# Kernel optimization log

Hardware: AMD Instinct MI355X
Metric: run time of the kernel (lower is better)

The kernel has to match this reference:

```python
import jax, jax.numpy as jnp
import numpy as np
from functools import partial

BIG = 1e9  # placeholder squared distance for 'no surface voxel here'


def _surface(fg):
    """Boundary voxels: foreground with at least one 4-neighbor background (image border counts as background)."""
    p = jnp.pad(fg, 1)  # pads with False
    interior = p[:-2, 1:-1] & p[2:, 1:-1] & p[1:-1, :-2] & p[1:-1, 2:]
    return fg & ~interior


def _edt(mask):
    """Exact Euclidean distance transform (unit spacing, matching spacing_mm=(1,1,1)).
    Separable two-pass: 1D squared distance along rows, then combine along columns.
    mask: [H, W] bool -> dist: [H, W] float32 distance to nearest True voxel."""
    H, W = mask.shape
    i = jnp.arange(H, dtype=jnp.float32)
    j = jnp.arange(W, dtype=jnp.float32)
    d1 = (i[:, None] - i[None, :]) ** 2                      # [H, H]
    pen = jnp.where(mask, 0.0, BIG).astype(jnp.float32)      # [H, W]
    g = jnp.min(d1[:, :, None] + pen[None, :, :], axis=1)    # [H, W] (min over source row i')
    d2 = (j[:, None] - j[None, :]) ** 2                      # [W, W]
    f = jnp.min(g[:, None, :] + d2[None, :, :], axis=2)      # [H, W] (min over source col j')
    return jnp.sqrt(f)


def _percentile(d, mask, pct):
    """pct-percentile of d over voxels where mask is True (inf if mask empty)."""
    vals = jnp.sort(jnp.where(mask, d, jnp.inf).ravel())
    n = jnp.sum(mask)
    idx = jnp.clip(jnp.ceil(pct / 100.0 * n.astype(jnp.float32)).astype(jnp.int32) - 1,
                   0, vals.size - 1)
    return jnp.where(n > 0, vals[idx], jnp.inf)


def _pair_hd(pred_m, gt_m):
    """Robust Hausdorff (100th and 95th percentile) between surfaces of two binary masks."""
    sp = _surface(pred_m)
    sg = _surface(gt_m)
    dt_to_pred = _edt(sp)  # distance of every voxel to pred surface
    dt_to_gt = _edt(sg)    # distance of every voxel to gt surface

    def robust(p):
        return jnp.maximum(_percentile(dt_to_pred, sg, p),   # gt -> pred
                           _percentile(dt_to_gt, sp, p))     # pred -> gt

    return jnp.stack([robust(100.0), robust(95.0)])  # [2]


def _forward(logits, target):
    num_classes = logits.shape[1]
    probs = jax.nn.softmax(logits, axis=1)
    pred = jnp.argmax(probs, axis=1)  # [B, H, W]
    classes = jnp.arange(1, num_classes)  # include_background=False -> drop class 0
    pred_oh = pred[:, None, :, :] == classes[None, :, None, None]    # [B, Cfg, H, W] bool
    tgt_oh = target[:, None, :, :] == classes[None, :, None, None]   # [B, Cfg, H, W] bool

    def per_image(args):
        pm, tm = args  # each [Cfg, H, W]
        return jax.vmap(_pair_hd)(pm, tm)  # [Cfg, 2]

    res = jax.lax.map(per_image, (pred_oh, tgt_oh))  # [B, Cfg, 2]
    # average='micro': mean over all (batch, class) pairs
    return jnp.mean(res, axis=(0, 1))  # [2] = (hd100, hd95)


def setup_inputs() -> dict:
    key = jax.random.key(0)
    k1, k2 = jax.random.split(key)
    B, C, H, W = 8, 4, 192, 192
    logits = jax.random.normal(k1, (B, C, H, W), dtype=jnp.float32)
    target = jax.random.randint(k2, (B, H, W), 0, C, dtype=jnp.int64)
    return {"logits": logits, "target": target}


def reference(logits, target):
    return _forward(logits, target)
```

## Files before the change

### kernel.cpp

```cpp
#include <hip/hip_runtime.h>
#include <hip/hip_bf16.h>
#include <math.h>
#include <stdint.h>
#include <limits.h>

#define BB 8
#define NC 4
#define HH 192
#define WW 192
#define HWP (HH * WW)
#define NPAIR 24
#define NPD 48
#define NWRD 576
#define NCHUNK 16
#define WPC (NWRD / NCHUNK)
#define BIGI 1000000000

typedef unsigned long long u64;

__global__ void k_prep(const float* __restrict__ logits, const int* __restrict__ target,
                       u64* __restrict__ fgbits) {
    int idx = blockIdx.x * 256 + threadIdx.x;
    int b = idx / HWP;
    int p = idx - b * HWP;
    const float* base = logits + (size_t)b * NC * HWP + p;
    float l0 = base[0], l1 = base[HWP], l2 = base[2 * HWP], l3 = base[3 * HWP];
    int pred = 0; float best = l0;
    if (l1 > best) { best = l1; pred = 1; }
    if (l2 > best) { best = l2; pred = 2; }
    if (l3 > best) { best = l3; pred = 3; }
    int t = target[(size_t)b * HWP + p];
    int lane = threadIdx.x & 63;
    int g = p >> 6;
#pragma unroll
    for (int cls = 1; cls <= 3; ++cls) {
        u64 mp = __ballot(pred == cls);
        u64 mt = __ballot(t == cls);
        if (lane == 0) {
            int pair = b * 3 + (cls - 1);
            fgbits[(size_t)(pair * 2 + 0) * NWRD + g] = mp;
            fgbits[(size_t)(pair * 2 + 1) * NWRD + g] = mt;
        }
    }
}

__device__ __forceinline__ u64 surf_word(const u64* F, int i, int k) {
    u64 r0 = F[i * 3], r1 = F[i * 3 + 1], r2 = F[i * 3 + 2];
    u64 r = F[i * 3 + k];
    u64 u = (i > 0) ? F[(i - 1) * 3 + k] : 0ull;
    u64 d = (i < HH - 1) ? F[(i + 1) * 3 + k] : 0ull;
    u64 lf, rt;
    if (k == 0)      { lf = r0 << 1;                rt = (r0 >> 1) | (r1 << 63); }
    else if (k == 1) { lf = (r1 << 1) | (r0 >> 63); rt = (r1 >> 1) | (r2 << 63); }
    else             { lf = (r2 << 1) | (r1 >> 63); rt = r2 >> 1; }
    return r & ~(u & d & lf & rt);
}

__device__ __forceinline__ int rowdist(const u64* w, int j) {
    int qw = j >> 6, qb = j & 63;
    int dr = INT_MAX, dl = INT_MAX;
    u64 m = w[qw] & (~0ull << qb);
    if (m) dr = ((qw << 6) + __ffsll(m) - 1) - j;
    else {
        for (int k = qw + 1; k < 3; ++k)
            if (w[k]) { dr = ((k << 6) + __ffsll(w[k]) - 1) - j; break; }
    }
    u64 ml = w[qw] & (~0ull >> (63 - qb));
    if (ml) dl = j - ((qw << 6) + 63 - __clzll((long long)ml));
    else {
        for (int k = qw - 1; k >= 0; --k)
            if (w[k]) { dl = j - ((k << 6) + 63 - __clzll((long long)w[k])); break; }
    }
    return min(dl, dr);
}

__global__ __launch_bounds__(256) void k_query(const u64* __restrict__ fgbits,
                        int* __restrict__ list, int* __restrict__ cnt) {
    int chunk = blockIdx.x, pd = blockIdx.y, qpd = pd ^ 1;
    int tid = threadIdx.x;
    __shared__ u64 sF[NWRD];
    __shared__ u64 sG[NWRD];
    __shared__ u64 sS[NWRD];
    __shared__ uint16_t qb[WPC * 64];
    __shared__ int wcnt[WPC + 1];
    __shared__ int sbase;

    for (int t = tid; t < NWRD; t += 256) {
        sF[t] = fgbits[(size_t)pd * NWRD + t];
        sG[t] = fgbits[(size_t)qpd * NWRD + t];
    }
    __syncthreads();

    for (int w = tid; w < NWRD; w += 256) sS[w] = surf_word(sF, w / 3, w % 3);

    u64 myq = 0;
    if (tid < WPC) {
        int w = chunk * WPC + tid;
        myq = surf_word(sG, w / 3, w % 3);
        wcnt[tid] = __popcll(myq);
    }
    __syncthreads();
    if (tid == 0) {
        int acc = 0;
        for (int w = 0; w < WPC; ++w) { int c = wcnt[w]; wcnt[w] = acc; acc += c; }
        wcnt[WPC] = acc;
        sbase = atomicAdd(&cnt[pd], acc);
    }
    __syncthreads();
    if (tid < WPC) {
        int w = chunk * WPC + tid;
        int i = w / 3, k = w % 3;
        int off = wcnt[tid];
        u64 m = myq;
        while (m) { int bi = __ffsll(m) - 1; m &= m - 1; qb[off++] = (uint16_t)((i << 8) | (k * 64 + bi)); }
    }
    __syncthreads();

    int nq = wcnt[WPC], base = sbase;
    for (int q = tid; q < nq; q += 256) {
        int e = qb[q];
        int qi = e >> 8, qj = e & 255;
        int best = BIGI;
        for (int s = 0; s < HH; ++s) {
            if (s * s >= best) break;
            int r = qi - s;
            if (r >= 0) {
                int dj = rowdist(sS + r * 3, qj);
                if (dj != INT_MAX) best = min(best, s * s + dj * dj);
            }
            r = qi + s;
            if (s > 0 && r < HH) {
                int dj = rowdist(sS + r * 3, qj);
                if (dj != INT_MAX) best = min(best, s * s + dj * dj);
            }
        }
        list[(size_t)pd * HWP + base + q] = best;
    }
}

__global__ __launch_bounds__(1024) void k_pick(const int* __restrict__ list,
                        const int* __restrict__ cnt, float* __restrict__ res) {
    int pd = blockIdx.x, tid = threadIdx.x;
    int n = cnt[pd];
    const int* L = list + (size_t)pd * HWP;
    int lv[16];
#pragma unroll
    for (int t = 0; t < 16; ++t) {
        int k = tid + t * 1024;
        lv[t] = (k < n) ? L[k] : INT_MAX;
    }
    __shared__ int sw[16];
    __shared__ int stot;

    int lmax = -1;
#pragma unroll
    for (int t = 0; t < 16; ++t) if (lv[t] != INT_MAX) lmax = max(lmax, lv[t]);
    for (int off = 32; off; off >>= 1) lmax = max(lmax, __shfl_down(lmax, off));
    if ((tid & 63) == 0) sw[tid >> 6] = lmax;
    __syncthreads();
    if (tid == 0) { int m = -1; for (int w = 0; w < 16; ++w) m = max(m, sw[w]); stot = m; }
    __syncthreads();
    int vmax = stot;
    __syncthreads();

    int kk;
    { float kf = ceilf(0.95f * (float)n); kk = (int)kf; if (kk < 1) kk = 1; if (kk > n) kk = n; }

    int lo = 0, hi = min(vmax, 72962);
    while (lo < hi) {
        int mid = (lo + hi) >> 1;
        int c = 0;
#pragma unroll
        for (int t = 0; t < 16; ++t) if (lv[t] <= mid) c++;
        for (int off = 32; off; off >>= 1) c += __shfl_down(c, off);
        if ((tid & 63) == 0) sw[tid >> 6] = c;
        __syncthreads();
        if (tid == 0) { int s = 0; for (int w = 0; w < 16; ++w) s += sw[w]; stot = s; }
        __syncthreads();
        if (stot >= kk) hi = mid; else lo = mid + 1;
        __syncthreads();
    }
    int c = 0;
#pragma unroll
    for (int t = 0; t < 16; ++t) if (lv[t] <= lo) c++;
    for (int off = 32; off; off >>= 1) c += __shfl_down(c, off);
    if ((tid & 63) == 0) sw[tid >> 6] = c;
    __syncthreads();
    if (tid == 0) {
        int s = 0; for (int w = 0; w < 16; ++w) s += sw[w];
        int v95 = (n > 0 && s >= kk) ? lo : BIGI;
        float r100, r95;
        if (n == 0) { r100 = INFINITY; r95 = INFINITY; }
        else { r100 = sqrtf((float)vmax); r95 = sqrtf((float)v95); }
        res[pd * 2 + 0] = r100;
        res[pd * 2 + 1] = r95;
    }
}

__global__ void k_final(const float* __restrict__ res, float* __restrict__ out) {
    int tid = threadIdx.x;
    float v100 = 0.0f, v95 = 0.0f;
    if (tid < NPAIR) {
        v100 = fmaxf(res[tid * 4 + 0], res[tid * 4 + 2]);
        v95  = fmaxf(res[tid * 4 + 1], res[tid * 4 + 3]);
    }
    for (int off = 32; off; off >>= 1) {
        v100 += __shfl_down(v100, off);
        v95  += __shfl_down(v95, off);
    }
    if (tid == 0) {
        out[0] = v100 / (float)NPAIR;
        out[1] = v95 / (float)NPAIR;
    }
}

extern "C" void kernel_launch(void* const* d_in, const int* in_sizes, int n_in,
                              void* d_out, int out_size, void* d_ws, size_t ws_size,
                              hipStream_t stream) {
    const float* logits = (const float*)d_in[0];
    const int* target = (const int*)d_in[1];
    float* out = (float*)d_out;

    uint8_t* ws = (uint8_t*)d_ws;
    u64*   fgbits = (u64*)ws;
    int*   list   = (int*)(ws + 221184);
    int*   cnt    = (int*)(ws + 7299072);
    float* res    = (float*)(ws + 7299264);

    hipMemsetAsync(cnt, 0, NPD * sizeof(int), stream);

    k_prep<<<(BB * HWP) / 256, 256, 0, stream>>>(logits, target, fgbits);
    k_query<<<dim3(NCHUNK, NPD), 256, 0, stream>>>(fgbits, list, cnt);
    k_pick<<<NPD, 1024, 0, stream>>>(list, cnt, res);
    k_final<<<1, 64, 0, stream>>>(res, out);
}
```

Before: 82.28 us.

## Fuse all stages into one cooperative persistent kernel with grid syncs

Replaces the memset and four separate launches with a single cooperative kernel of 768 blocks that runs the prep, query, percentile-pick and final-reduce stages, separated by grid.sync. The goal is to remove launch gaps and the memset. The pick stage now uses 256-thread blocks and stages the per-pair distance list in shared memory, falling back to global memory beyond the cap. Risks are the cost of grid-wide barriers, fewer threads working in the pick phase, and occupancy limits from the larger shared-memory union needed to keep 768 blocks co-resident.

After: 289.1 us. 3.51x slower.

```diff
diff --git a/kernel.cpp b/kernel.cpp
--- a/kernel.cpp
+++ b/kernel.cpp
@@ -1,8 +1,11 @@
 #include <hip/hip_runtime.h>
+#include <hip/hip_cooperative_groups.h>
 #include <hip/hip_bf16.h>
 #include <math.h>
 #include <stdint.h>
 #include <limits.h>
+
+namespace cg = cooperative_groups;
 
 #define BB 8
 #define NC 4
@@ -14,35 +17,25 @@
 #define NWRD 576
 #define NCHUNK 16
 #define WPC (NWRD / NCHUNK)
+#define GB 768
+#define PCAP 12288
 #define BIGI 1000000000
 
 typedef unsigned long long u64;
 
-__global__ void k_prep(const float* __restrict__ logits, const int* __restrict__ target,
-                       u64* __restrict__ fgbits) {
-    int idx = blockIdx.x * 256 + threadIdx.x;
-    int b = idx / HWP;
-    int p = idx - b * HWP;
-    const float* base = logits + (size_t)b * NC * HWP + p;
-    float l0 = base[0], l1 = base[HWP], l2 = base[2 * HWP], l3 = base[3 * HWP];
-    int pred = 0; float best = l0;
-    if (l1 > best) { best = l1; pred = 1; }
-    if (l2 > best) { best = l2; pred = 2; }
-    if (l3 > best) { best = l3; pred = 3; }
-    int t = target[(size_t)b * HWP + p];
-    int lane = threadIdx.x & 63;
-    int g = p >> 6;
-#pragma unroll
-    for (int cls = 1; cls <= 3; ++cls) {
-        u64 mp = __ballot(pred == cls);
-        u64 mt = __ballot(t == cls);
-        if (lane == 0) {
-            int pair = b * 3 + (cls - 1);
-            fgbits[(size_t)(pair * 2 + 0) * NWRD + g] = mp;
-            fgbits[(size_t)(pair * 2 + 1) * NWRD + g] = mt;
-        }
-    }
-}
+struct P2 {
+    u64 sF[NWRD];
+    u64 sG[NWRD];
+    u64 sS[NWRD];
+    uint16_t qb[WPC * 64];
+    int wcnt[WPC + 1];
+    int sbase;
+};
+struct P3 {
+    int vals[PCAP];
+    int sw[4];
+};
+union ShU { P2 p2; P3 p3; };
 
 __device__ __forceinline__ u64 surf_word(const u64* F, int i, int k) {
     u64 r0 = F[i * 3], r1 = F[i * 3 + 1], r2 = F[i * 3 + 2];
@@ -57,15 +50,15 @@
 }
 
 __device__ __forceinline__ int rowdist(const u64* w, int j) {
-    int qw = j >> 6, qb = j & 63;
+    int qw = j >> 6, qb2 = j & 63;
     int dr = INT_MAX, dl = INT_MAX;
-    u64 m = w[qw] & (~0ull << qb);
+    u64 m = w[qw] & (~0ull << qb2);
     if (m) dr = ((qw << 6) + __ffsll(m) - 1) - j;
     else {
         for (int k = qw + 1; k < 3; ++k)
             if (w[k]) { dr = ((k << 6) + __ffsll(w[k]) - 1) - j; break; }
     }
-    u64 ml = w[qw] & (~0ull >> (63 - qb));
+    u64 ml = w[qw] & (~0ull >> (63 - qb2));
     if (ml) dl = j - ((qw << 6) + 63 - __clzll((long long)ml));
     else {
         for (int k = qw - 1; k >= 0; --k)
@@ -74,143 +67,174 @@
     return min(dl, dr);
 }
 
-__global__ __launch_bounds__(256) void k_query(const u64* __restrict__ fgbits,
-                        int* __restrict__ list, int* __restrict__ cnt) {
-    int chunk = blockIdx.x, pd = blockIdx.y, qpd = pd ^ 1;
-    int tid = threadIdx.x;
-    __shared__ u64 sF[NWRD];
-    __shared__ u64 sG[NWRD];
-    __shared__ u64 sS[NWRD];
-    __shared__ uint16_t qb[WPC * 64];
-    __shared__ int wcnt[WPC + 1];
-    __shared__ int sbase;
-
-    for (int t = tid; t < NWRD; t += 256) {
-        sF[t] = fgbits[(size_t)pd * NWRD + t];
-        sG[t] = fgbits[(size_t)qpd * NWRD + t];
-    }
-    __syncthreads();
-
-    for (int w = tid; w < NWRD; w += 256) sS[w] = surf_word(sF, w / 3, w % 3);
-
-    u64 myq = 0;
-    if (tid < WPC) {
-        int w = chunk * WPC + tid;
-        myq = surf_word(sG, w / 3, w % 3);
-        wcnt[tid] = __popcll(myq);
-    }
-    __syncthreads();
-    if (tid == 0) {
-        int acc = 0;
-        for (int w = 0; w < WPC; ++w) { int c = wcnt[w]; wcnt[w] = acc; acc += c; }
-        wcnt[WPC] = acc;
-        sbase = atomicAdd(&cnt[pd], acc);
-    }
-    __syncthreads();
-    if (tid < WPC) {
-        int w = chunk * WPC + tid;
-        int i = w / 3, k = w % 3;
-        int off = wcnt[tid];
-        u64 m = myq;
-        while (m) { int bi = __ffsll(m) - 1; m &= m - 1; qb[off++] = (uint16_t)((i << 8) | (k * 64 + bi)); }
-    }
-    __syncthreads();
-
-    int nq = wcnt[WPC], base = sbase;
-    for (int q = tid; q < nq; q += 256) {
-        int e = qb[q];
-        int qi = e >> 8, qj = e & 255;
-        int best = BIGI;
-        for (int s = 0; s < HH; ++s) {
-            if (s * s >= best) break;
-            int r = qi - s;
-            if (r >= 0) {
-                int dj = rowdist(sS + r * 3, qj);
-                if (dj != INT_MAX) best = min(best, s * s + dj * dj);
+__device__ __forceinline__ void prep_word(int w, int lane, const float* __restrict__ logits,
+                                          const int* __restrict__ target, u64* __restrict__ fgbits) {
+    int b = w / NWRD;
+    int g = w - b * NWRD;
+    int p = (g << 6) + lane;
+    const float* base = logits + (size_t)b * NC * HWP + p;
+    float l0 = base[0], l1 = base[HWP], l2 = base[2 * HWP], l3 = base[3 * HWP];
+    int pred = 0; float best = l0;
+    if (l1 > best) { best = l1; pred = 1; }
+    if (l2 > best) { best = l2; pred = 2; }
+    if (l3 > best) { best = l3; pred = 3; }
+    int t = target[(size_t)b * HWP + p];
+#pragma unroll
+    for (int cls = 1; cls <= 3; ++cls) {
+        u64 mp = __ballot(pred == cls);
+        u64 mt = __ballot(t == cls);
+        if (lane == 0) {
+            int pair = b * 3 + (cls - 1);
+            fgbits[(size_t)(pair * 2 + 0) * NWRD + g] = mp;
+            fgbits[(size_t)(pair * 2 + 1) * NWRD + g] = mt;
+        }
+    }
+}
+
+__device__ __forceinline__ int block_reduce_add(int v, int* sw, int tid) {
+    for (int off = 32; off; off >>= 1) v += __shfl_down(v, off);
+    if ((tid & 63) == 0) sw[tid >> 6] = v;
+    __syncthreads();
+    int r = sw[0] + sw[1] + sw[2] + sw[3];
+    __syncthreads();
+    return r;
+}
+__device__ __forceinline__ int block_reduce_max(int v, int* sw, int tid) {
+    for (int off = 32; off; off >>= 1) v = max(v, __shfl_down(v, off));
+    if ((tid & 63) == 0) sw[tid >> 6] = v;
+    __syncthreads();
+    int r = max(max(sw[0], sw[1]), max(sw[2], sw[3]));
+    __syncthreads();
+    return r;
+}
+
+__global__ __launch_bounds__(256, 3) void k_all(const float* __restrict__ logits,
+                        const int* __restrict__ target, u64* __restrict__ fgbits,
+                        int* __restrict__ list, int* __restrict__ cnt,
+                        float* __restrict__ res, float* __restrict__ out) {
+    cg::grid_group grid = cg::this_grid();
+    __shared__ ShU sh;
+    int tid = threadIdx.x, bid = blockIdx.x;
+
+    if (bid == 0 && tid < NPD) cnt[tid] = 0;
+    {
+        int gtid = bid * 256 + tid;
+        int w0 = gtid >> 6, lane = gtid & 63;
+        prep_word(w0, lane, logits, target, fgbits);
+        int w1 = w0 + 3072;
+        if (w1 < BB * NWRD) prep_word(w1, lane, logits, target, fgbits);
+    }
+    grid.sync();
+
+    {
+        int pd = bid >> 4, chunk = bid & 15, qpd = pd ^ 1;
+        for (int t = tid; t < NWRD; t += 256) {
+            sh.p2.sF[t] = fgbits[(size_t)pd * NWRD + t];
+            sh.p2.sG[t] = fgbits[(size_t)qpd * NWRD + t];
+        }
+        __syncthreads();
+        for (int w = tid; w < NWRD; w += 256) sh.p2.sS[w] = surf_word(sh.p2.sF, w / 3, w % 3);
+
+        u64 myq = 0;
+        if (tid < WPC) {
+            int w = chunk * WPC + tid;
+            myq = surf_word(sh.p2.sG, w / 3, w % 3);
+            sh.p2.wcnt[tid] = __popcll(myq);
+        }
+        __syncthreads();
+        if (tid == 0) {
+            int acc = 0;
+            for (int w = 0; w < WPC; ++w) { int c = sh.p2.wcnt[w]; sh.p2.wcnt[w] = acc; acc += c; }
+            sh.p2.wcnt[WPC] = acc;
+            sh.p2.sbase = atomicAdd(&cnt[pd], acc);
+        }
+        __syncthreads();
+        if (tid < WPC) {
+            int w = chunk * WPC + tid;
+            int i = w / 3, k = w % 3;
+            int off = sh.p2.wcnt[tid];
+            u64 m = myq;
+            while (m) { int bi = __ffsll(m) - 1; m &= m - 1; sh.p2.qb[off++] = (uint16_t)((i << 8) | (k * 64 + bi)); }
+        }
+        __syncthreads();
+
+        int nq = sh.p2.wcnt[WPC], base = sh.p2.sbase;
+        for (int q = tid; q < nq; q += 256) {
+            int e = sh.p2.qb[q];
+            int qi = e >> 8, qj = e & 255;
+            int best = BIGI;
+            for (int s = 0; s < HH; ++s) {
+                if (s * s >= best) break;
+                int r = qi - s;
+                if (r >= 0) {
+                    int dj = rowdist(sh.p2.sS + r * 3, qj);
+                    if (dj != INT_MAX) best = min(best, s * s + dj * dj);
+                }
+                r = qi + s;
+                if (s > 0 && r < HH) {
+                    int dj = rowdist(sh.p2.sS + r * 3, qj);
+                    if (dj != INT_MAX) best = min(best, s * s + dj * dj);
+                }
             }
-            r = qi + s;
-            if (s > 0 && r < HH) {
-                int dj = rowdist(sS + r * 3, qj);
-                if (dj != INT_MAX) best = min(best, s * s + dj * dj);
+            list[(size_t)pd * HWP + base + q] = best;
+        }
+    }
+    grid.sync();
+
+    if (bid < NPD) {
+        int pd = bid;
+        int n = cnt[pd];
+        const int* L = list + (size_t)pd * HWP;
+        int m = min(n, PCAP);
+        for (int k = tid; k < m; k += 256) sh.p3.vals[k] = L[k];
+        __syncthreads();
+
+        int lmax = -1;
+        for (int k = tid; k < m; k += 256) lmax = max(lmax, sh.p3.vals[k]);
+        for (int k = PCAP + tid; k < n; k += 256) lmax = max(lmax, L[k]);
+        int vmax = block_reduce_max(lmax, sh.p3.sw, tid);
+
+        if (n == 0) {
+            if (tid == 0) { res[pd * 2 + 0] = INFINITY; res[pd * 2 + 1] = INFINITY; }
+        } else {
+            int kk;
+            { float kf = ceilf(0.95f * (float)n); kk = (int)kf; if (kk < 1) kk = 1; if (kk > n) kk = n; }
+            int lo = 0, hi = min(vmax, 72962);
+            while (lo < hi) {
+                int mid = (lo + hi) >> 1;
+                int c = 0;
+                for (int k = tid; k < m; k += 256) if (sh.p3.vals[k] <= mid) c++;
+                for (int k = PCAP + tid; k < n; k += 256) if (L[k] <= mid) c++;
+                int tot = block_reduce_add(c, sh.p3.sw, tid);
+                if (tot >= kk) hi = mid; else lo = mid + 1;
             }
-        }
-        list[(size_t)pd * HWP + base + q] = best;
-    }
-}
-
-__global__ __launch_bounds__(1024) void k_pick(const int* __restrict__ list,
-                        const int* __restrict__ cnt, float* __restrict__ res) {
-    int pd = blockIdx.x, tid = threadIdx.x;
-    int n = cnt[pd];
-    const int* L = list + (size_t)pd * HWP;
-    int lv[16];
-#pragma unroll
-    for (int t = 0; t < 16; ++t) {
-        int k = tid + t * 1024;
-        lv[t] = (k < n) ? L[k] : INT_MAX;
-    }
-    __shared__ int sw[16];
-    __shared__ int stot;
-
-    int lmax = -1;
-#pragma unroll
-    for (int t = 0; t < 16; ++t) if (lv[t] != INT_MAX) lmax = max(lmax, lv[t]);
-    for (int off = 32; off; off >>= 1) lmax = max(lmax, __shfl_down(lmax, off));
-    if ((tid & 63) == 0) sw[tid >> 6] = lmax;
-    __syncthreads();
-    if (tid == 0) { int m = -1; for (int w = 0; w < 16; ++w) m = max(m, sw[w]); stot = m; }
-    __syncthreads();
-    int vmax = stot;
-    __syncthreads();
-
-    int kk;
-    { float kf = ceilf(0.95f * (float)n); kk = (int)kf; if (kk < 1) kk = 1; if (kk > n) kk = n; }
-
-    int lo = 0, hi = min(vmax, 72962);
-    while (lo < hi) {
-        int mid = (lo + hi) >> 1;
-        int c = 0;
-#pragma unroll
-        for (int t = 0; t < 16; ++t) if (lv[t] <= mid) c++;
-        for (int off = 32; off; off >>= 1) c += __shfl_down(c, off);
-        if ((tid & 63) == 0) sw[tid >> 6] = c;
-        __syncthreads();
-        if (tid == 0) { int s = 0; for (int w = 0; w < 16; ++w) s += sw[w]; stot = s; }
-        __syncthreads();
-        if (stot >= kk) hi = mid; else lo = mid + 1;
-        __syncthreads();
-    }
-    int c = 0;
-#pragma unroll
-    for (int t = 0; t < 16; ++t) if (lv[t] <= lo) c++;
-    for (int off = 32; off; off >>= 1) c += __shfl_down(c, off);
-    if ((tid & 63) == 0) sw[tid >> 6] = c;
-    __syncthreads();
-    if (tid == 0) {
-        int s = 0; for (int w = 0; w < 16; ++w) s += sw[w];
-        int v95 = (n > 0 && s >= kk) ? lo : BIGI;
-        float r100, r95;
-        if (n == 0) { r100 = INFINITY; r95 = INFINITY; }
-        else { r100 = sqrtf((float)vmax); r95 = sqrtf((float)v95); }
-        res[pd * 2 + 0] = r100;
-        res[pd * 2 + 1] = r95;
-    }
-}
-
-__global__ void k_final(const float* __restrict__ res, float* __restrict__ out) {
-    int tid = threadIdx.x;
-    float v100 = 0.0f, v95 = 0.0f;
-    if (tid < NPAIR) {
-        v100 = fmaxf(res[tid * 4 + 0], res[tid * 4 + 2]);
-        v95  = fmaxf(res[tid * 4 + 1], res[tid * 4 + 3]);
-    }
-    for (int off = 32; off; off >>= 1) {
-        v100 += __shfl_down(v100, off);
-        v95  += __shfl_down(v95, off);
-    }
-    if (tid == 0) {
-        out[0] = v100 / (float)NPAIR;
-        out[1] = v95 / (float)NPAIR;
+            int c = 0;
+            for (int k = tid; k < m; k += 256) if (sh.p3.vals[k] <= lo) c++;
+            for (int k = PCAP + tid; k < n; k += 256) if (L[k] <= lo) c++;
+            int tot = block_reduce_add(c, sh.p3.sw, tid);
+            if (tid == 0) {
+                int v95 = (tot >= kk) ? lo : BIGI;
+                res[pd * 2 + 0] = sqrtf((float)vmax);
+                res[pd * 2 + 1] = sqrtf((float)v95);
+            }
+        }
+    }
+    grid.sync();
+
+    if (bid == 0 && tid < 64) {
+        float v100 = 0.0f, v95 = 0.0f;
+        if (tid < NPAIR) {
+            v100 = fmaxf(res[tid * 4 + 0], res[tid * 4 + 2]);
+            v95  = fmaxf(res[tid * 4 + 1], res[tid * 4 + 3]);
+        }
+        for (int off = 32; off; off >>= 1) {
+            v100 += __shfl_down(v100, off);
+            v95  += __shfl_down(v95, off);
+        }
+        if (tid == 0) {
+            out[0] = v100 / (float)NPAIR;
+            out[1] = v95 / (float)NPAIR;
+        }
     }
 }
 
@@ -227,10 +251,7 @@
     int*   cnt    = (int*)(ws + 7299072);
     float* res    = (float*)(ws + 7299264);
 
-    hipMemsetAsync(cnt, 0, NPD * sizeof(int), stream);
-
-    k_prep<<<(BB * HWP) / 256, 256, 0, stream>>>(logits, target, fgbits);
-    k_query<<<dim3(NCHUNK, NPD), 256, 0, stream>>>(fgbits, list, cnt);
-    k_pick<<<NPD, 1024, 0, stream>>>(list, cnt, res);
-    k_final<<<1, 64, 0, stream>>>(res, out);
-}
+    void* args[] = { (void*)&logits, (void*)&target, (void*)&fgbits, (void*)&list,
+                     (void*)&cnt, (void*)&res, (void*)&out };
+    hipLaunchCooperativeKernel((void*)k_all, dim3(GB), dim3(256), args, 0, stream);
+}
```

## Fuse surface query and percentile pick into one block-per-pair kernel

Applied to the files above, without the earlier changes.

Merges the query kernel (16 chunks x 48 pair-directions) and the pick kernel into a single kernel with one 1024-thread block per pair-direction. Query coordinates are compacted in shared memory and the distances stay in registers for the percentile search, with a global spill path when there are more than 16384 query points. This removes a launch, the memset, the atomic counter and the global round-trip of the distance list. In exchange, parallelism for the nearest-surface search drops from 768 blocks to 48.

Measured after the change: 90.02 us. 1.09x slower.

```diff
diff --git a/kernel.cpp b/kernel.cpp
--- a/kernel.cpp
+++ b/kernel.cpp
@@ -12,8 +12,7 @@
 #define NPAIR 24
 #define NPD 48
 #define NWRD 576
-#define NCHUNK 16
-#define WPC (NWRD / NCHUNK)
+#define PCAP 16384
 #define BIGI 1000000000
 
 typedef unsigned long long u64;
@@ -57,15 +56,15 @@
 }
 
 __device__ __forceinline__ int rowdist(const u64* w, int j) {
-    int qw = j >> 6, qb = j & 63;
+    int qw = j >> 6, qb2 = j & 63;
     int dr = INT_MAX, dl = INT_MAX;
-    u64 m = w[qw] & (~0ull << qb);
+    u64 m = w[qw] & (~0ull << qb2);
     if (m) dr = ((qw << 6) + __ffsll(m) - 1) - j;
     else {
         for (int k = qw + 1; k < 3; ++k)
             if (w[k]) { dr = ((k << 6) + __ffsll(w[k]) - 1) - j; break; }
     }
-    u64 ml = w[qw] & (~0ull >> (63 - qb));
+    u64 ml = w[qw] & (~0ull >> (63 - qb2));
     if (ml) dl = j - ((qw << 6) + 63 - __clzll((long long)ml));
     else {
         for (int k = qw - 1; k >= 0; --k)
@@ -74,126 +73,133 @@
     return min(dl, dr);
 }
 
-__global__ __launch_bounds__(256) void k_query(const u64* __restrict__ fgbits,
-                        int* __restrict__ list, int* __restrict__ cnt) {
-    int chunk = blockIdx.x, pd = blockIdx.y, qpd = pd ^ 1;
-    int tid = threadIdx.x;
+__device__ __forceinline__ int nearest2(const u64* sS, int qi, int qj) {
+    int best = BIGI;
+    for (int s = 0; s < HH; ++s) {
+        if (s * s >= best) break;
+        int r = qi - s;
+        if (r >= 0) {
+            int dj = rowdist(sS + r * 3, qj);
+            if (dj != INT_MAX) best = min(best, s * s + dj * dj);
+        }
+        r = qi + s;
+        if (s > 0 && r < HH) {
+            int dj = rowdist(sS + r * 3, qj);
+            if (dj != INT_MAX) best = min(best, s * s + dj * dj);
+        }
+    }
+    return best;
+}
+
+__global__ __launch_bounds__(1024) void k_main(const u64* __restrict__ fgbits,
+                        uint16_t* __restrict__ spillq, int* __restrict__ spillv,
+                        float* __restrict__ res) {
+    int pd = blockIdx.x, qpd = pd ^ 1;
+    int tid = threadIdx.x, lane = tid & 63, wid = tid >> 6;
     __shared__ u64 sF[NWRD];
     __shared__ u64 sG[NWRD];
     __shared__ u64 sS[NWRD];
-    __shared__ uint16_t qb[WPC * 64];
-    __shared__ int wcnt[WPC + 1];
-    __shared__ int sbase;
-
-    for (int t = tid; t < NWRD; t += 256) {
-        sF[t] = fgbits[(size_t)pd * NWRD + t];
-        sG[t] = fgbits[(size_t)qpd * NWRD + t];
-    }
-    __syncthreads();
-
-    for (int w = tid; w < NWRD; w += 256) sS[w] = surf_word(sF, w / 3, w % 3);
-
-    u64 myq = 0;
-    if (tid < WPC) {
-        int w = chunk * WPC + tid;
-        myq = surf_word(sG, w / 3, w % 3);
-        wcnt[tid] = __popcll(myq);
-    }
+    __shared__ uint16_t qb[PCAP];
+    __shared__ int swt[16], swo[16];
+    __shared__ int sn, stot, sw[16];
+
+    if (tid < NWRD) {
+        sF[tid] = fgbits[(size_t)pd * NWRD + tid];
+        sG[tid] = fgbits[(size_t)qpd * NWRD + tid];
+    }
+    __syncthreads();
+
+    u64 myq = 0; int c = 0;
+    if (tid < NWRD) {
+        sS[tid] = surf_word(sF, tid / 3, tid % 3);
+        myq = surf_word(sG, tid / 3, tid % 3);
+        c = __popcll(myq);
+    }
+    int inc = c;
+    for (int off = 1; off < 64; off <<= 1) { int t = __shfl_up(inc, off); if (lane >= off) inc += t; }
+    if (lane == 63) swt[wid] = inc;
     __syncthreads();
     if (tid == 0) {
         int acc = 0;
-        for (int w = 0; w < WPC; ++w) { int c = wcnt[w]; wcnt[w] = acc; acc += c; }
-        wcnt[WPC] = acc;
-        sbase = atomicAdd(&cnt[pd], acc);
-    }
-    __syncthreads();
-    if (tid < WPC) {
-        int w = chunk * WPC + tid;
-        int i = w / 3, k = w % 3;
-        int off = wcnt[tid];
+        for (int w = 0; w < 16; ++w) { swo[w] = acc; acc += swt[w]; }
+        sn = acc;
+    }
+    __syncthreads();
+    int n = sn;
+
+    if (c > 0) {
+        int off = swo[wid] + inc - c;
+        int i = tid / 3, k = tid % 3;
         u64 m = myq;
-        while (m) { int bi = __ffsll(m) - 1; m &= m - 1; qb[off++] = (uint16_t)((i << 8) | (k * 64 + bi)); }
-    }
-    __syncthreads();
-
-    int nq = wcnt[WPC], base = sbase;
-    for (int q = tid; q < nq; q += 256) {
-        int e = qb[q];
-        int qi = e >> 8, qj = e & 255;
-        int best = BIGI;
-        for (int s = 0; s < HH; ++s) {
-            if (s * s >= best) break;
-            int r = qi - s;
-            if (r >= 0) {
-                int dj = rowdist(sS + r * 3, qj);
-                if (dj != INT_MAX) best = min(best, s * s + dj * dj);
-            }
-            r = qi + s;
-            if (s > 0 && r < HH) {
-                int dj = rowdist(sS + r * 3, qj);
-                if (dj != INT_MAX) best = min(best, s * s + dj * dj);
-            }
-        }
-        list[(size_t)pd * HWP + base + q] = best;
-    }
-}
-
-__global__ __launch_bounds__(1024) void k_pick(const int* __restrict__ list,
-                        const int* __restrict__ cnt, float* __restrict__ res) {
-    int pd = blockIdx.x, tid = threadIdx.x;
-    int n = cnt[pd];
-    const int* L = list + (size_t)pd * HWP;
+        while (m) {
+            int bi = __ffsll(m) - 1; m &= m - 1;
+            uint16_t coord = (uint16_t)((i << 8) | (k * 64 + bi));
+            if (off < PCAP) qb[off] = coord;
+            else spillq[(size_t)pd * HWP + off - PCAP] = coord;
+            ++off;
+        }
+    }
+    __syncthreads();
+
+    int m2 = min(n, PCAP);
     int lv[16];
 #pragma unroll
     for (int t = 0; t < 16; ++t) {
         int k = tid + t * 1024;
-        lv[t] = (k < n) ? L[k] : INT_MAX;
-    }
-    __shared__ int sw[16];
-    __shared__ int stot;
+        lv[t] = INT_MAX;
+        if (k < m2) { int e = qb[k]; lv[t] = nearest2(sS, e >> 8, e & 255); }
+    }
+    for (int k = PCAP + tid; k < n; k += 1024) {
+        int e = spillq[(size_t)pd * HWP + k - PCAP];
+        spillv[(size_t)pd * HWP + k - PCAP] = nearest2(sS, e >> 8, e & 255);
+    }
+    __syncthreads();
 
     int lmax = -1;
 #pragma unroll
     for (int t = 0; t < 16; ++t) if (lv[t] != INT_MAX) lmax = max(lmax, lv[t]);
+    for (int k = PCAP + tid; k < n; k += 1024) lmax = max(lmax, spillv[(size_t)pd * HWP + k - PCAP]);
     for (int off = 32; off; off >>= 1) lmax = max(lmax, __shfl_down(lmax, off));
-    if ((tid & 63) == 0) sw[tid >> 6] = lmax;
-    __syncthreads();
-    if (tid == 0) { int m = -1; for (int w = 0; w < 16; ++w) m = max(m, sw[w]); stot = m; }
+    if (lane == 0) sw[wid] = lmax;
+    __syncthreads();
+    if (tid == 0) { int v = -1; for (int w = 0; w < 16; ++w) v = max(v, sw[w]); stot = v; }
     __syncthreads();
     int vmax = stot;
     __syncthreads();
 
+    if (n == 0) {
+        if (tid == 0) { res[pd * 2 + 0] = INFINITY; res[pd * 2 + 1] = INFINITY; }
+        return;
+    }
     int kk;
     { float kf = ceilf(0.95f * (float)n); kk = (int)kf; if (kk < 1) kk = 1; if (kk > n) kk = n; }
-
     int lo = 0, hi = min(vmax, 72962);
     while (lo < hi) {
         int mid = (lo + hi) >> 1;
-        int c = 0;
-#pragma unroll
-        for (int t = 0; t < 16; ++t) if (lv[t] <= mid) c++;
-        for (int off = 32; off; off >>= 1) c += __shfl_down(c, off);
-        if ((tid & 63) == 0) sw[tid >> 6] = c;
+        int cc = 0;
+#pragma unroll
+        for (int t = 0; t < 16; ++t) if (lv[t] <= mid) cc++;
+        for (int k = PCAP + tid; k < n; k += 1024) if (spillv[(size_t)pd * HWP + k - PCAP] <= mid) cc++;
+        for (int off = 32; off; off >>= 1) cc += __shfl_down(cc, off);
+        if (lane == 0) sw[wid] = cc;
         __syncthreads();
         if (tid == 0) { int s = 0; for (int w = 0; w < 16; ++w) s += sw[w]; stot = s; }
         __syncthreads();
         if (stot >= kk) hi = mid; else lo = mid + 1;
         __syncthreads();
     }
-    int c = 0;
-#pragma unroll
-    for (int t = 0; t < 16; ++t) if (lv[t] <= lo) c++;
-    for (int off = 32; off; off >>= 1) c += __shfl_down(c, off);
-    if ((tid & 63) == 0) sw[tid >> 6] = c;
+    int cc = 0;
+#pragma unroll
+    for (int t = 0; t < 16; ++t) if (lv[t] <= lo) cc++;
+    for (int k = PCAP + tid; k < n; k += 1024) if (spillv[(size_t)pd * HWP + k - PCAP] <= lo) cc++;
+    for (int off = 32; off; off >>= 1) cc += __shfl_down(cc, off);
+    if (lane == 0) sw[wid] = cc;
     __syncthreads();
     if (tid == 0) {
         int s = 0; for (int w = 0; w < 16; ++w) s += sw[w];
-        int v95 = (n > 0 && s >= kk) ? lo : BIGI;
-        float r100, r95;
-        if (n == 0) { r100 = INFINITY; r95 = INFINITY; }
-        else { r100 = sqrtf((float)vmax); r95 = sqrtf((float)v95); }
-        res[pd * 2 + 0] = r100;
-        res[pd * 2 + 1] = r95;
+        int v95 = (s >= kk) ? lo : BIGI;
+        res[pd * 2 + 0] = sqrtf((float)vmax);
+        res[pd * 2 + 1] = sqrtf((float)v95);
     }
 }
 
@@ -222,15 +228,12 @@
     float* out = (float*)d_out;
 
     uint8_t* ws = (uint8_t*)d_ws;
-    u64*   fgbits = (u64*)ws;
-    int*   list   = (int*)(ws + 221184);
-    int*   cnt    = (int*)(ws + 7299072);
-    float* res    = (float*)(ws + 7299264);
-
-    hipMemsetAsync(cnt, 0, NPD * sizeof(int), stream);
+    u64*      fgbits = (u64*)ws;
+    uint16_t* spillq = (uint16_t*)(ws + 221184);
+    int*      spillv = (int*)(ws + 3760128);
+    float*    res    = (float*)(ws + 10838016);
 
     k_prep<<<(BB * HWP) / 256, 256, 0, stream>>>(logits, target, fgbits);
-    k_query<<<dim3(NCHUNK, NPD), 256, 0, stream>>>(fgbits, list, cnt);
-    k_pick<<<NPD, 1024, 0, stream>>>(list, cnt, res);
+    k_main<<<NPD, 1024, 0, stream>>>(fgbits, spillq, spillv, res);
     k_final<<<1, 64, 0, stream>>>(res, out);
 }
```

## Replace per-pair distance list and binary search with histogram percentile selection

Applied to the files above, without the earlier changes.

The query kernel now builds a shared-memory histogram of squared distances below 4096 and merges it into a global per-pair histogram. Larger values go to an overflow list. The selection kernel finds max and the 95th percentile from a prefix scan over the histogram, and binary-searches only the overflow values when needed. The zeroing of the histogram and overflow counters moves into the prep kernel, which removes the memset launch and the 1024-thread bisection over full lists. The cost is extra shared and global atomics in the query kernel and a larger shared-memory footprint per block.

Measured after the change: 75.50 us. -8.2%, faster.

```diff
diff --git a/kernel.cpp b/kernel.cpp
--- a/kernel.cpp
+++ b/kernel.cpp
@@ -14,13 +14,20 @@
 #define NWRD 576
 #define NCHUNK 16
 #define WPC (NWRD / NCHUNK)
+#define NBIN 4096
 #define BIGI 1000000000
 
 typedef unsigned long long u64;
 
 __global__ void k_prep(const float* __restrict__ logits, const int* __restrict__ target,
-                       u64* __restrict__ fgbits) {
+                       u64* __restrict__ fgbits, unsigned* __restrict__ ghist,
+                       int* __restrict__ ovfcnt, int* __restrict__ ovfmax) {
     int idx = blockIdx.x * 256 + threadIdx.x;
+    if (idx < NPD * NBIN) ghist[idx] = 0;
+    if (blockIdx.x == 1151) {
+        if (threadIdx.x < NPD) ovfcnt[threadIdx.x] = 0;
+        else if (threadIdx.x >= 64 && threadIdx.x < 64 + NPD) ovfmax[threadIdx.x - 64] = 0;
+    }
     int b = idx / HWP;
     int p = idx - b * HWP;
     const float* base = logits + (size_t)b * NC * HWP + p;
@@ -57,15 +64,15 @@
 }
 
 __device__ __forceinline__ int rowdist(const u64* w, int j) {
-    int qw = j >> 6, qb = j & 63;
+    int qw = j >> 6, qb2 = j & 63;
     int dr = INT_MAX, dl = INT_MAX;
-    u64 m = w[qw] & (~0ull << qb);
+    u64 m = w[qw] & (~0ull << qb2);
     if (m) dr = ((qw << 6) + __ffsll(m) - 1) - j;
     else {
         for (int k = qw + 1; k < 3; ++k)
             if (w[k]) { dr = ((k << 6) + __ffsll(w[k]) - 1) - j; break; }
     }
-    u64 ml = w[qw] & (~0ull >> (63 - qb));
+    u64 ml = w[qw] & (~0ull >> (63 - qb2));
     if (ml) dl = j - ((qw << 6) + 63 - __clzll((long long)ml));
     else {
         for (int k = qw - 1; k >= 0; --k)
@@ -75,22 +82,23 @@
 }
 
 __global__ __launch_bounds__(256) void k_query(const u64* __restrict__ fgbits,
-                        int* __restrict__ list, int* __restrict__ cnt) {
+                        unsigned* __restrict__ ghist, int* __restrict__ ovfval,
+                        int* __restrict__ ovfcnt, int* __restrict__ ovfmax) {
     int chunk = blockIdx.x, pd = blockIdx.y, qpd = pd ^ 1;
     int tid = threadIdx.x;
     __shared__ u64 sF[NWRD];
     __shared__ u64 sG[NWRD];
     __shared__ u64 sS[NWRD];
     __shared__ uint16_t qb[WPC * 64];
+    __shared__ unsigned shist[NBIN];
     __shared__ int wcnt[WPC + 1];
-    __shared__ int sbase;
 
     for (int t = tid; t < NWRD; t += 256) {
         sF[t] = fgbits[(size_t)pd * NWRD + t];
         sG[t] = fgbits[(size_t)qpd * NWRD + t];
     }
-    __syncthreads();
-
+    for (int t = tid; t < NBIN; t += 256) shist[t] = 0;
+    __syncthreads();
     for (int w = tid; w < NWRD; w += 256) sS[w] = surf_word(sF, w / 3, w % 3);
 
     u64 myq = 0;
@@ -104,7 +112,6 @@
         int acc = 0;
         for (int w = 0; w < WPC; ++w) { int c = wcnt[w]; wcnt[w] = acc; acc += c; }
         wcnt[WPC] = acc;
-        sbase = atomicAdd(&cnt[pd], acc);
     }
     __syncthreads();
     if (tid < WPC) {
@@ -116,7 +123,7 @@
     }
     __syncthreads();
 
-    int nq = wcnt[WPC], base = sbase;
+    int nq = wcnt[WPC];
     for (int q = tid; q < nq; q += 256) {
         int e = qb[q];
         int qi = e >> 8, qj = e & 255;
@@ -134,66 +141,94 @@
                 if (dj != INT_MAX) best = min(best, s * s + dj * dj);
             }
         }
-        list[(size_t)pd * HWP + base + q] = best;
-    }
-}
-
-__global__ __launch_bounds__(1024) void k_pick(const int* __restrict__ list,
-                        const int* __restrict__ cnt, float* __restrict__ res) {
-    int pd = blockIdx.x, tid = threadIdx.x;
-    int n = cnt[pd];
-    const int* L = list + (size_t)pd * HWP;
-    int lv[16];
-#pragma unroll
-    for (int t = 0; t < 16; ++t) {
-        int k = tid + t * 1024;
-        lv[t] = (k < n) ? L[k] : INT_MAX;
-    }
-    __shared__ int sw[16];
-    __shared__ int stot;
-
-    int lmax = -1;
-#pragma unroll
-    for (int t = 0; t < 16; ++t) if (lv[t] != INT_MAX) lmax = max(lmax, lv[t]);
-    for (int off = 32; off; off >>= 1) lmax = max(lmax, __shfl_down(lmax, off));
-    if ((tid & 63) == 0) sw[tid >> 6] = lmax;
-    __syncthreads();
-    if (tid == 0) { int m = -1; for (int w = 0; w < 16; ++w) m = max(m, sw[w]); stot = m; }
-    __syncthreads();
-    int vmax = stot;
-    __syncthreads();
-
+        if (best < NBIN) {
+            atomicAdd(&shist[best], 1u);
+        } else {
+            int ix = atomicAdd(&ovfcnt[pd], 1);
+            ovfval[(size_t)pd * HWP + ix] = best;
+            atomicMax(&ovfmax[pd], best);
+        }
+    }
+    __syncthreads();
+    for (int bin = tid; bin < NBIN; bin += 256)
+        if (shist[bin]) atomicAdd(&ghist[pd * NBIN + bin], shist[bin]);
+}
+
+__global__ __launch_bounds__(256) void k_sel(const unsigned* __restrict__ ghist,
+                        const int* __restrict__ ovfval, const int* __restrict__ ovfcnt,
+                        const int* __restrict__ ovfmax, float* __restrict__ res) {
+    int pd = blockIdx.x, tid = threadIdx.x, lane = tid & 63, wid = tid >> 6;
+    __shared__ int swt[4];
+    __shared__ int sred[4];
+    __shared__ int sv95;
+    const unsigned* H = ghist + pd * NBIN;
+
+    unsigned c[16];
+    int s_t = 0;
+#pragma unroll
+    for (int u = 0; u < 16; ++u) { c[u] = H[tid * 16 + u]; s_t += (int)c[u]; }
+
+    int inc = s_t;
+    for (int off = 1; off < 64; off <<= 1) { int t = __shfl_up(inc, off); if (lane >= off) inc += t; }
+    if (lane == 63) swt[wid] = inc;
+    __syncthreads();
+    int woff = 0;
+    for (int w = 0; w < wid; ++w) woff += swt[w];
+    int total = swt[0] + swt[1] + swt[2] + swt[3];
+    int base = woff + inc - s_t;
+
+    int novf = ovfcnt[pd];
+    int n = total + novf;
+
+    int mybin = -1;
+#pragma unroll
+    for (int u = 0; u < 16; ++u) if (c[u]) mybin = tid * 16 + u;
+    for (int off = 32; off; off >>= 1) mybin = max(mybin, __shfl_down(mybin, off));
+    if (lane == 0) sred[wid] = mybin;
+    __syncthreads();
+    int vmax = max(max(sred[0], sred[1]), max(sred[2], sred[3]));
+    if (novf > 0) vmax = max(vmax, ovfmax[pd]);
+
+    if (n == 0) {
+        if (tid == 0) { res[pd * 2 + 0] = INFINITY; res[pd * 2 + 1] = INFINITY; }
+        return;
+    }
     int kk;
     { float kf = ceilf(0.95f * (float)n); kk = (int)kf; if (kk < 1) kk = 1; if (kk > n) kk = n; }
 
-    int lo = 0, hi = min(vmax, 72962);
-    while (lo < hi) {
-        int mid = (lo + hi) >> 1;
-        int c = 0;
-#pragma unroll
-        for (int t = 0; t < 16; ++t) if (lv[t] <= mid) c++;
-        for (int off = 32; off; off >>= 1) c += __shfl_down(c, off);
-        if ((tid & 63) == 0) sw[tid >> 6] = c;
+    if (kk <= total) {
+        if (base < kk && kk <= base + s_t) {
+            int cum = base;
+#pragma unroll
+            for (int u = 0; u < 16; ++u) {
+                cum += (int)c[u];
+                if (cum >= kk) { sv95 = tid * 16 + u; break; }
+            }
+        }
         __syncthreads();
-        if (tid == 0) { int s = 0; for (int w = 0; w < 16; ++w) s += sw[w]; stot = s; }
-        __syncthreads();
-        if (stot >= kk) hi = mid; else lo = mid + 1;
-        __syncthreads();
-    }
-    int c = 0;
-#pragma unroll
-    for (int t = 0; t < 16; ++t) if (lv[t] <= lo) c++;
-    for (int off = 32; off; off >>= 1) c += __shfl_down(c, off);
-    if ((tid & 63) == 0) sw[tid >> 6] = c;
-    __syncthreads();
-    if (tid == 0) {
-        int s = 0; for (int w = 0; w < 16; ++w) s += sw[w];
-        int v95 = (n > 0 && s >= kk) ? lo : BIGI;
-        float r100, r95;
-        if (n == 0) { r100 = INFINITY; r95 = INFINITY; }
-        else { r100 = sqrtf((float)vmax); r95 = sqrtf((float)v95); }
-        res[pd * 2 + 0] = r100;
-        res[pd * 2 + 1] = r95;
+        if (tid == 0) {
+            res[pd * 2 + 0] = sqrtf((float)vmax);
+            res[pd * 2 + 1] = sqrtf((float)sv95);
+        }
+    } else {
+        int r = kk - total;
+        const int* OV = ovfval + (size_t)pd * HWP;
+        int lo = NBIN, hi = vmax;
+        while (lo < hi) {
+            int mid = lo + ((hi - lo) >> 1);
+            int cc = 0;
+            for (int k = tid; k < novf; k += 256) if (OV[k] <= mid) cc++;
+            for (int off = 32; off; off >>= 1) cc += __shfl_down(cc, off);
+            if (lane == 0) sred[wid] = cc;
+            __syncthreads();
+            int tot = sred[0] + sred[1] + sred[2] + sred[3];
+            __syncthreads();
+            if (tot >= r) hi = mid; else lo = mid + 1;
+        }
+        if (tid == 0) {
+            res[pd * 2 + 0] = sqrtf((float)vmax);
+            res[pd * 2 + 1] = sqrtf((float)lo);
+        }
     }
 }
 
@@ -222,15 +257,15 @@
     float* out = (float*)d_out;
 
     uint8_t* ws = (uint8_t*)d_ws;
-    u64*   fgbits = (u64*)ws;
-    int*   list   = (int*)(ws + 221184);
-    int*   cnt    = (int*)(ws + 7299072);
-    float* res    = (float*)(ws + 7299264);
-
-    hipMemsetAsync(cnt, 0, NPD * sizeof(int), stream);
-
-    k_prep<<<(BB * HWP) / 256, 256, 0, stream>>>(logits, target, fgbits);
-    k_query<<<dim3(NCHUNK, NPD), 256, 0, stream>>>(fgbits, list, cnt);
-    k_pick<<<NPD, 1024, 0, stream>>>(list, cnt, res);
+    u64*      fgbits = (u64*)ws;
+    unsigned* ghist  = (unsigned*)(ws + 221184);
+    int*      ovfval = (int*)(ws + 1007616);
+    int*      ovfcnt = (int*)(ws + 8085504);
+    int*      ovfmax = (int*)(ws + 8085696);
+    float*    res    = (float*)(ws + 8085888);
+
+    k_prep<<<(BB * HWP) / 256, 256, 0, stream>>>(logits, target, fgbits, ghist, ovfcnt, ovfmax);
+    k_query<<<dim3(NCHUNK, NPD), 256, 0, stream>>>(fgbits, ghist, ovfval, ovfcnt, ovfmax);
+    k_sel<<<NPD, 256, 0, stream>>>(ghist, ovfval, ovfcnt, ovfmax, res);
     k_final<<<1, 64, 0, stream>>>(res, out);
 }
```
